# Performance work log

Measured on AMD Instinct MI355X. Metric: run time of the kernel, lower is better.

The kernel has to match this reference:

```python
import jax, jax.numpy as jnp
import numpy as np

B, N, N_IN, N_H = 8192, 16, 512, 256
NEG_ROUND = 1
MARGIN = 0.5
EPS = 1e-6  # torch F.pairwise_distance default eps


def setup_inputs() -> dict:
    key = jax.random.key(0)
    k0, k1, k2, k3 = jax.random.split(key, 4)
    seq1 = jax.random.normal(k0, (B, N, N_IN), dtype=jnp.float32)
    adj = jax.random.uniform(k1, (B, N, N), dtype=jnp.float32)
    # GCN linear (bias=False), xavier_uniform on [n_h, n_in] == same bound for [n_in, n_h]
    gx = float(np.sqrt(6.0 / (N_IN + N_H)))
    W_gcn = jax.random.uniform(k2, (N_IN, N_H), dtype=jnp.float32, minval=-gx, maxval=gx)
    b_gcn = jnp.zeros((N_H,), dtype=jnp.float32)  # Simple_GCN self.bias, init 0
    prelu_a = jnp.asarray(0.25, dtype=jnp.float32)  # nn.PReLU default
    bx = float(np.sqrt(6.0 / (N_H + N_H)))
    W_bil = jax.random.uniform(k3, (N_H, N_H), dtype=jnp.float32, minval=-bx, maxval=bx)
    b_bil = jnp.zeros((), dtype=jnp.float32)
    return {"seq1": seq1, "adj": adj, "W_gcn": W_gcn, "b_gcn": b_gcn,
            "prelu_a": prelu_a, "W_bil": W_bil, "b_bil": b_bil}


def reference(seq1, adj, W_gcn, b_gcn, prelu_a, W_bil, b_bil):
    # Simple_GCN: linear -> adjacency aggregate -> bias -> PReLU
    seq_fts = jnp.einsum('bnf,fh->bnh', seq1, W_gcn)           # [B,N,n_h]
    h1 = jnp.einsum('bnm,bmh->bnh', adj, seq_fts) + b_gcn      # bmm(adj, seq_fts)+bias
    h1 = jnp.where(h1 >= 0, h1, prelu_a * h1)                  # PReLU

    # avg readout over context nodes; last node is the target
    c = jnp.mean(h1[:, :-1, :], axis=1)                        # [B,n_h]
    h_mv = h1[:, -1, :]                                        # [B,n_h]

    def bilinear(x1, x2):  # nn.Bilinear(n_h, n_h, 1)
        return jnp.einsum('bi,ij,bj->b', x1, W_bil, x2)[:, None] + b_bil  # [B,1]

    scs = [bilinear(h_mv, c)]
    c_mi = c
    for _ in range(NEG_ROUND):  # fixed small loop, mirrors torch shift
        c_mi = jnp.concatenate([c_mi[-2:-1, :], c_mi[:-1, :]], axis=0)
        scs.append(bilinear(h_mv, c_mi))

    pos_dis = jnp.linalg.norm(h_mv - c + EPS, axis=-1)         # F.pairwise_distance
    neg_dis = jnp.linalg.norm(h_mv - c_mi + EPS, axis=-1)

    logits = jnp.concatenate(scs, axis=0)                      # [(1+NEG)*B, 1]
    # MarginRankingLoss(margin, reduction='none') with y=-1:
    # max(0, -y*(x1-x2)+margin) = max(0, (pos-neg)+margin)
    loss2 = jnp.maximum(0.0, (pos_dis - neg_dis) + MARGIN)     # [B]
    return (logits, loss2)
```

## Files before the change

kernel.cpp:

```cpp
#include <hip/hip_runtime.h>
#include <stdint.h>

typedef float f32x4 __attribute__((ext_vector_type(4)));
typedef __bf16 bfrag __attribute__((ext_vector_type(8)));
typedef unsigned short us4 __attribute__((ext_vector_type(4)));

__device__ __forceinline__ unsigned short f2bf(float f) {
  unsigned u = __float_as_uint(f);
  u += 0x7fff + ((u >> 16) & 1);
  return (unsigned short)(u >> 16);
}
__device__ __forceinline__ float bf2f(unsigned short s) {
  return __uint_as_float(((unsigned)s) << 16);
}

typedef __attribute__((address_space(3))) void lds_vp;
typedef __attribute__((address_space(1))) void gl_vp;
__device__ __forceinline__ void gload16(const void* g, void* l) {
  __builtin_amdgcn_global_load_lds((const gl_vp*)g, (lds_vp*)l, 16, 0, 0);
}

__global__ __launch_bounds__(256)
void conv_w_k(const float* __restrict__ Wg, const float* __restrict__ Wb,
              unsigned short* __restrict__ WgT, unsigned short* __restrict__ WbT) {
  int i = blockIdx.x * 256 + threadIdx.x;
  if (i < 512 * 256) { int k = i >> 8, c = i & 255; WgT[c * 512 + k] = f2bf(Wg[i]); }
  if (i < 256 * 256) { int k = i >> 8, c = i & 255; WbT[c * 256 + k] = f2bf(Wb[i]); }
}

__global__ __launch_bounds__(512, 4)
void fused1_k(const float* __restrict__ A, const unsigned short* __restrict__ Bt,
              const float* __restrict__ adj, const float* __restrict__ b_gcn,
              const float* __restrict__ prelu_a,
              float* __restrict__ Cout, float* __restrict__ Hmv) {
  __shared__ __align__(16) char sm[65536];
  const int t = threadIdx.x;
  const int lane = t & 63;
  const int wid = t >> 6;
  const int wm = wid >> 2, wn = wid & 3;
  const int lrow = lane & 15, lgrp = lane >> 4;
  const int wg = blockIdx.x;

  const float* gA = A + (size_t)(wg * 128 + (t >> 2)) * 512 + (t & 3) * 8;
  const int aw_off = t * 16;

  int aoff[4], boff[4];
#pragma unroll
  for (int m = 0; m < 4; m++) {
    int arow = wm * 64 + m * 16 + lrow;
    aoff[m] = arow * 64 + lgrp * 16;
  }
#pragma unroll
  for (int n = 0; n < 4; n++) {
    int bcol = wn * 64 + n * 16 + lrow;
    boff[n] = 8192 + bcol * 64 + ((lgrp ^ ((bcol ^ (bcol >> 2)) & 3)) << 4);
  }

  f32x4 acc[4][4];
#pragma unroll
  for (int m = 0; m < 4; m++)
#pragma unroll
    for (int n = 0; n < 4; n++) acc[m][n] = (f32x4)0.0f;

#define STAGE_B(buf, kc)                                                       \
  {                                                                            \
    _Pragma("unroll")                                                          \
    for (int i = 0; i < 2; i++) {                                              \
      int c = i * 512 + t;                                                     \
      int col = c >> 2, s = c & 3;                                             \
      int sp = s ^ ((col ^ (col >> 2)) & 3);                                   \
      gload16(Bt + (size_t)col * 512 + (kc) * 32 + sp * 8, (buf) + 8192 + c * 16); \
    }                                                                          \
  }

#define COMPUTE(cur)                                                           \
  {                                                                            \
    bfrag bf[4], af[4];                                                        \
    _Pragma("unroll")                                                          \
    for (int n = 0; n < 4; n++) bf[n] = *(const bfrag*)((cur) + boff[n]);      \
    _Pragma("unroll")                                                          \
    for (int m = 0; m < 4; m++) af[m] = *(const bfrag*)((cur) + aoff[m]);      \
    _Pragma("unroll")                                                          \
    for (int m = 0; m < 4; m++)                                                \
      _Pragma("unroll")                                                        \
      for (int n = 0; n < 4; n++)                                              \
        acc[m][n] = __builtin_amdgcn_mfma_f32_16x16x32_bf16(af[m], bf[n], acc[m][n], 0, 0, 0); \
  }

  {
    STAGE_B(sm, 0);
    f32x4 a0 = *(const f32x4*)(gA);
    f32x4 a1 = *(const f32x4*)(gA + 4);
    bfrag w;
    w[0] = (__bf16)a0.x; w[1] = (__bf16)a0.y; w[2] = (__bf16)a0.z; w[3] = (__bf16)a0.w;
    w[4] = (__bf16)a1.x; w[5] = (__bf16)a1.y; w[6] = (__bf16)a1.z; w[7] = (__bf16)a1.w;
    *(bfrag*)(sm + aw_off) = w;
    asm volatile("s_waitcnt vmcnt(0)" ::: "memory");
    asm volatile("s_waitcnt lgkmcnt(0)" ::: "memory");
    __builtin_amdgcn_s_barrier();
    asm volatile("" ::: "memory");
  }

  for (int kc = 0; kc < 15; ++kc) {
    char* cur = sm + (kc & 1) * 24576;
    char* nxt = sm + ((kc + 1) & 1) * 24576;
    f32x4 a0 = *(const f32x4*)(gA + (kc + 1) * 32);
    f32x4 a1 = *(const f32x4*)(gA + (kc + 1) * 32 + 4);
    STAGE_B(nxt, kc + 1);

    COMPUTE(cur);

    bfrag w;
    w[0] = (__bf16)a0.x; w[1] = (__bf16)a0.y; w[2] = (__bf16)a0.z; w[3] = (__bf16)a0.w;
    w[4] = (__bf16)a1.x; w[5] = (__bf16)a1.y; w[6] = (__bf16)a1.z; w[7] = (__bf16)a1.w;
    *(bfrag*)(nxt + aw_off) = w;
    asm volatile("s_waitcnt vmcnt(0)" ::: "memory");
    asm volatile("s_waitcnt lgkmcnt(0)" ::: "memory");
    __builtin_amdgcn_s_barrier();
    asm volatile("" ::: "memory");
  }
  COMPUTE(sm + 24576);
  __builtin_amdgcn_s_barrier();
  asm volatile("" ::: "memory");
#undef STAGE_B
#undef COMPUTE

  unsigned short* sf = (unsigned short*)sm;
#pragma unroll
  for (int m = 0; m < 4; m++) {
    int row = wm * 64 + m * 16 + lgrp * 4;
#pragma unroll
    for (int n = 0; n < 4; n++) {
      int col = wn * 64 + n * 16 + lrow;
#pragma unroll
      for (int rr = 0; rr < 4; rr++)
        sf[(row + rr) * 256 + col] = f2bf(acc[m][n][rr]);
    }
  }
  asm volatile("s_waitcnt lgkmcnt(0)" ::: "memory");
  __builtin_amdgcn_s_barrier();
  asm volatile("" ::: "memory");

  const float pa = prelu_a[0];
  const f32x4 bg = *(const f32x4*)(b_gcn + lane * 4);
  f32x4 sfr[16];
#pragma unroll
  for (int mm = 0; mm < 16; mm++) {
    us4 q = *(const us4*)(sf + (wid * 16 + mm) * 256 + lane * 4);
    f32x4 v;
    v.x = bf2f(q.x); v.y = bf2f(q.y); v.z = bf2f(q.z); v.w = bf2f(q.w);
    sfr[mm] = v;
  }
  const int b = wg * 8 + wid;
  const float* adjb = adj + (size_t)b * 256;
  f32x4 cacc = (f32x4)0.0f;
  f32x4 hmv = (f32x4)0.0f;
#pragma unroll
  for (int n = 0; n < 16; n++) {
    f32x4 a4 = (f32x4)0.0f;
#pragma unroll
    for (int m = 0; m < 16; m++) a4 += adjb[n * 16 + m] * sfr[m];
    a4 += bg;
    f32x4 hv;
    hv.x = a4.x >= 0.f ? a4.x : pa * a4.x;
    hv.y = a4.y >= 0.f ? a4.y : pa * a4.y;
    hv.z = a4.z >= 0.f ? a4.z : pa * a4.z;
    hv.w = a4.w >= 0.f ? a4.w : pa * a4.w;
    if (n < 15) cacc += hv; else hmv = hv;
  }
  cacc *= (1.0f / 15.0f);
  *(f32x4*)(Cout + (size_t)b * 256 + lane * 4) = cacc;
  *(f32x4*)(Hmv + (size_t)b * 256 + lane * 4) = hmv;
}

__device__ __forceinline__ void stage2(const float* __restrict__ A,
                                       const unsigned short* __restrict__ Bt,
                                       char* buf, int wg, int kc, int t) {
  {
    int c = t & 255;
    int row = c >> 3, s = c & 7;
    int sp = s ^ (((row & 3) << 1) | ((row >> 2) & 1));
    gload16(A + (size_t)(wg * 32 + row) * 256 + kc * 32 + sp * 4, buf + c * 16);
  }
#pragma unroll
  for (int i = 0; i < 2; i++) {
    int c = i * 512 + t;
    int col = c >> 2, s = c & 3;
    int sp = s ^ ((col ^ (col >> 2)) & 3);
    gload16(Bt + (size_t)col * 256 + kc * 32 + sp * 8, buf + 4096 + c * 16);
  }
}

__global__ __launch_bounds__(512)
void fused2_k(const float* __restrict__ A, const unsigned short* __restrict__ Bt,
              const float* __restrict__ C, const float* __restrict__ Hmv,
              const float* __restrict__ b_bil, float* __restrict__ out) {
  __shared__ __align__(16) char sm2[40960];
  const int t = threadIdx.x;
  const int lane = t & 63;
  const int wid = t >> 6;
  const int wm = wid >> 2, wn = wid & 3;
  const int lrow = lane & 15, lgrp = lane >> 4;
  const int wg = blockIdx.x;

  f32x4 acc[4];
#pragma unroll
  for (int n = 0; n < 4; n++) acc[n] = (f32x4)0.0f;

  stage2(A, Bt, sm2, wg, 0, t);

  for (int kc = 0; kc < 8; ++kc) {
    char* cur = sm2 + (kc & 1) * 20480;
    if (kc + 1 < 8) {
      stage2(A, Bt, sm2 + ((kc + 1) & 1) * 20480, wg, kc + 1, t);
      asm volatile("s_waitcnt vmcnt(3)" ::: "memory");
    } else {
      asm volatile("s_waitcnt vmcnt(0)" ::: "memory");
    }
    __builtin_amdgcn_s_barrier();
    asm volatile("" ::: "memory");

    bfrag bf[4];
#pragma unroll
    for (int n = 0; n < 4; n++) {
      int bcol = wn * 64 + n * 16 + lrow;
      int sB = (bcol ^ (bcol >> 2)) & 3;
      bf[n] = *(const bfrag*)(cur + 4096 + bcol * 64 + ((lgrp ^ sB) << 4));
    }
    {
      int arow = wm * 16 + lrow;
      int sw = ((arow & 3) << 1) | ((arow >> 2) & 1);
      f32x4 lo = *(const f32x4*)(cur + arow * 128 + (((lgrp * 2) ^ sw) << 4));
      f32x4 hi = *(const f32x4*)(cur + arow * 128 + (((lgrp * 2 + 1) ^ sw) << 4));
      bfrag am;
      am[0] = (__bf16)lo.x; am[1] = (__bf16)lo.y; am[2] = (__bf16)lo.z; am[3] = (__bf16)lo.w;
      am[4] = (__bf16)hi.x; am[5] = (__bf16)hi.y; am[6] = (__bf16)hi.z; am[7] = (__bf16)hi.w;
#pragma unroll
      for (int n = 0; n < 4; n++)
        acc[n] = __builtin_amdgcn_mfma_f32_16x16x32_bf16(am, bf[n], acc[n], 0, 0, 0);
    }
    __builtin_amdgcn_s_barrier();
    asm volatile("" ::: "memory");
  }

  float* sf = (float*)sm2;
  {
    int row = wm * 16 + lgrp * 4;
#pragma unroll
    for (int n = 0; n < 4; n++) {
      int col = wn * 64 + n * 16 + lrow;
#pragma unroll
      for (int rr = 0; rr < 4; rr++)
        sf[(row + rr) * 256 + col] = acc[n][rr];
    }
  }
  asm volatile("s_waitcnt lgkmcnt(0)" ::: "memory");
  __builtin_amdgcn_s_barrier();
  asm volatile("" ::: "memory");

  const float bb = b_bil[0];
#pragma unroll
  for (int r = 0; r < 4; ++r) {
    const int row = wid * 4 + r;
    const int b = wg * 32 + row;
    const int bp = (b == 0) ? 8190 : (b - 1);
    f32x4 tv = *(const f32x4*)(sf + row * 256 + lane * 4);
    f32x4 cv = *(const f32x4*)(C + (size_t)b * 256 + lane * 4);
    f32x4 cp = *(const f32x4*)(C + (size_t)bp * 256 + lane * 4);
    f32x4 hv = *(const f32x4*)(Hmv + (size_t)b * 256 + lane * 4);
    f32x4 d0 = hv - cv + 1e-6f;
    f32x4 d1 = hv - cp + 1e-6f;
    float s0 = tv.x * cv.x + tv.y * cv.y + tv.z * cv.z + tv.w * cv.w;
    float s1 = tv.x * cp.x + tv.y * cp.y + tv.z * cp.z + tv.w * cp.w;
    float p = d0.x * d0.x + d0.y * d0.y + d0.z * d0.z + d0.w * d0.w;
    float q = d1.x * d1.x + d1.y * d1.y + d1.z * d1.z + d1.w * d1.w;
#pragma unroll
    for (int m = 1; m < 64; m <<= 1) {
      s0 += __shfl_xor(s0, m, 64);
      s1 += __shfl_xor(s1, m, 64);
      p  += __shfl_xor(p, m, 64);
      q  += __shfl_xor(q, m, 64);
    }
    if (lane == 0) {
      out[b] = s0 + bb;
      out[8192 + b] = s1 + bb;
      out[16384 + b] = fmaxf(0.0f, sqrtf(p) - sqrtf(q) + 0.5f);
    }
  }
}

extern "C" void kernel_launch(void* const* d_in, const int* in_sizes, int n_in,
                              void* d_out, int out_size, void* d_ws, size_t ws_size,
                              hipStream_t stream) {
  (void)in_sizes; (void)n_in; (void)out_size; (void)ws_size;
  const float* seq1 = (const float*)d_in[0];
  const float* adj  = (const float*)d_in[1];
  const float* Wg   = (const float*)d_in[2];
  const float* bg   = (const float*)d_in[3];
  const float* pa   = (const float*)d_in[4];
  const float* Wb   = (const float*)d_in[5];
  const float* bb   = (const float*)d_in[6];
  float* out = (float*)d_out;
  char* ws = (char*)d_ws;

  unsigned short* WgT = (unsigned short*)(ws);
  unsigned short* WbT = (unsigned short*)(ws + 262144);
  float* C   = (float*)(ws + 524288);
  float* HMV = (float*)(ws + 524288 + 8388608);

  hipLaunchKernelGGL(conv_w_k, dim3(512), dim3(256), 0, stream, Wg, Wb, WgT, WbT);
  hipLaunchKernelGGL(fused1_k, dim3(1024), dim3(512), 0, stream,
                     seq1, WgT, adj, bg, pa, C, HMV);
  hipLaunchKernelGGL(fused2_k, dim3(256), dim3(512), 0, stream,
                     HMV, WbT, C, HMV, bb, out);
}
```

Before: 102.0 us.

## Enlarge GEMM tile to 256 rows with triple-buffered async fp32 A staging

The first fused kernel now handles 256 rows (16 batches) per block instead of 128. The fp32 activation tile is loaded straight into LDS with async global-to-LDS copies and converted to bf16 at fragment-read time, replacing register-staged conversion. A three-buffer pipeline with partial vmcnt waits replaces the double buffer that drained every iteration, and each wave computes a 64x128 tile, which raises MFMA work per B-fragment load. The cost is 144KB of dynamic shared memory, so only one block fits per CU and far fewer blocks are resident; the per-wave accumulators also double, which adds register pressure.

```diff
diff --git a/kernel.cpp b/kernel.cpp
--- a/kernel.cpp
+++ b/kernel.cpp
@@ -28,101 +28,104 @@
   if (i < 256 * 256) { int k = i >> 8, c = i & 255; WbT[c * 256 + k] = f2bf(Wb[i]); }
 }
 
-__global__ __launch_bounds__(512, 4)
+__global__ __launch_bounds__(512)
 void fused1_k(const float* __restrict__ A, const unsigned short* __restrict__ Bt,
               const float* __restrict__ adj, const float* __restrict__ b_gcn,
               const float* __restrict__ prelu_a,
               float* __restrict__ Cout, float* __restrict__ Hmv) {
-  __shared__ __align__(16) char sm[65536];
+  extern __shared__ __align__(16) char sm[];
   const int t = threadIdx.x;
   const int lane = t & 63;
   const int wid = t >> 6;
-  const int wm = wid >> 2, wn = wid & 3;
+  const int wm = wid >> 1, wn = wid & 1;
   const int lrow = lane & 15, lgrp = lane >> 4;
   const int wg = blockIdx.x;
 
-  const float* gA = A + (size_t)(wg * 128 + (t >> 2)) * 512 + (t & 3) * 8;
-  const int aw_off = t * 16;
-
-  int aoff[4], boff[4];
+  int aoff0[4], aoff1[4], boff[8];
 #pragma unroll
   for (int m = 0; m < 4; m++) {
     int arow = wm * 64 + m * 16 + lrow;
-    aoff[m] = arow * 64 + lgrp * 16;
-  }
-#pragma unroll
-  for (int n = 0; n < 4; n++) {
-    int bcol = wn * 64 + n * 16 + lrow;
-    boff[n] = 8192 + bcol * 64 + ((lgrp ^ ((bcol ^ (bcol >> 2)) & 3)) << 4);
-  }
-
-  f32x4 acc[4][4];
+    int s0 = (2 * lgrp) ^ (arow & 7);
+    int s1 = (2 * lgrp + 1) ^ (arow & 7);
+    aoff0[m] = arow * 128 + (s0 << 4);
+    aoff1[m] = arow * 128 + (s1 << 4);
+  }
+#pragma unroll
+  for (int n = 0; n < 8; n++) {
+    int bcol = wn * 128 + n * 16 + lrow;
+    boff[n] = 32768 + bcol * 64 + ((lgrp ^ ((bcol ^ (bcol >> 2)) & 3)) << 4);
+  }
+
+  f32x4 acc[4][8];
 #pragma unroll
   for (int m = 0; m < 4; m++)
 #pragma unroll
-    for (int n = 0; n < 4; n++) acc[m][n] = (f32x4)0.0f;
-
-#define STAGE_B(buf, kc)                                                       \
+    for (int n = 0; n < 8; n++) acc[m][n] = (f32x4)0.0f;
+
+#define STAGE(bufidx, kc)                                                      \
   {                                                                            \
     _Pragma("unroll")                                                          \
-    for (int i = 0; i < 2; i++) {                                              \
+    for (int i = 0; i < 4; i++) {             \
+      int c = i * 512 + t;                                                     \
+      int row = c >> 3, s = c & 7;                                             \
+      int sp = s ^ (row & 7);                                                  \
+      gload16(A + (size_t)(wg * 256 + row) * 512 + (kc) * 32 + sp * 4,         \
+              sm + (bufidx) * 49152 + c * 16);                                 \
+    }                                                                          \
+    _Pragma("unroll")                                                          \
+    for (int i = 0; i < 2; i++) {            \
       int c = i * 512 + t;                                                     \
       int col = c >> 2, s = c & 3;                                             \
       int sp = s ^ ((col ^ (col >> 2)) & 3);                                   \
-      gload16(Bt + (size_t)col * 512 + (kc) * 32 + sp * 8, (buf) + 8192 + c * 16); \
+      gload16(Bt + (size_t)col * 512 + (kc) * 32 + sp * 8,                     \
+              sm + (bufidx) * 49152 + 32768 + c * 16);                         \
     }                                                                          \
   }
 
-#define COMPUTE(cur)                                                           \
+#define COMPUTE(bufidx)                                                        \
   {                                                                            \
-    bfrag bf[4], af[4];                                                        \
+    const char* cur = sm + (bufidx) * 49152;                                   \
+    bfrag bf[8];                                                               \
     _Pragma("unroll")                                                          \
-    for (int n = 0; n < 4; n++) bf[n] = *(const bfrag*)((cur) + boff[n]);      \
+    for (int n = 0; n < 8; n++) bf[n] = *(const bfrag*)(cur + boff[n]);        \
     _Pragma("unroll")                                                          \
-    for (int m = 0; m < 4; m++) af[m] = *(const bfrag*)((cur) + aoff[m]);      \
-    _Pragma("unroll")                                                          \
-    for (int m = 0; m < 4; m++)                                                \
+    for (int m = 0; m < 4; m++) {                                              \
+      f32x4 lo = *(const f32x4*)(cur + aoff0[m]);                              \
+      f32x4 hi = *(const f32x4*)(cur + aoff1[m]);                              \
+      bfrag am;                                                                \
+      am[0] = (__bf16)lo.x; am[1] = (__bf16)lo.y;                              \
+      am[2] = (__bf16)lo.z; am[3] = (__bf16)lo.w;                              \
+      am[4] = (__bf16)hi.x; am[5] = (__bf16)hi.y;                              \
+      am[6] = (__bf16)hi.z; am[7] = (__bf16)hi.w;                              \
       _Pragma("unroll")                                                        \
-      for (int n = 0; n < 4; n++)                                              \
-        acc[m][n] = __builtin_amdgcn_mfma_f32_16x16x32_bf16(af[m], bf[n], acc[m][n], 0, 0, 0); \
-  }
-
-  {
-    STAGE_B(sm, 0);
-    f32x4 a0 = *(const f32x4*)(gA);
-    f32x4 a1 = *(const f32x4*)(gA + 4);
-    bfrag w;
-    w[0] = (__bf16)a0.x; w[1] = (__bf16)a0.y; w[2] = (__bf16)a0.z; w[3] = (__bf16)a0.w;
-    w[4] = (__bf16)a1.x; w[5] = (__bf16)a1.y; w[6] = (__bf16)a1.z; w[7] = (__bf16)a1.w;
-    *(bfrag*)(sm + aw_off) = w;
-    asm volatile("s_waitcnt vmcnt(0)" ::: "memory");
-    asm volatile("s_waitcnt lgkmcnt(0)" ::: "memory");
+      for (int n = 0; n < 8; n++)                                              \
+        acc[m][n] = __builtin_amdgcn_mfma_f32_16x16x32_bf16(am, bf[n], acc[m][n], 0, 0, 0); \
+    }                                                                          \
+  }
+
+  STAGE(0, 0);
+  STAGE(1, 1);
+  asm volatile("s_waitcnt vmcnt(6)" ::: "memory");
+  __builtin_amdgcn_s_barrier();
+  asm volatile("" ::: "memory");
+
+#pragma unroll
+  for (int p = 0; p < 16; ++p) {
+    if (p < 14) {
+      STAGE((p + 2) % 3, p + 2);
+      asm volatile("s_waitcnt vmcnt(12)" ::: "memory");
+    } else if (p == 14) {
+      asm volatile("s_waitcnt vmcnt(6)" ::: "memory");
+    } else {
+      asm volatile("s_waitcnt vmcnt(0)" ::: "memory");
+    }
     __builtin_amdgcn_s_barrier();
     asm volatile("" ::: "memory");
-  }
-
-  for (int kc = 0; kc < 15; ++kc) {
-    char* cur = sm + (kc & 1) * 24576;
-    char* nxt = sm + ((kc + 1) & 1) * 24576;
-    f32x4 a0 = *(const f32x4*)(gA + (kc + 1) * 32);
-    f32x4 a1 = *(const f32x4*)(gA + (kc + 1) * 32 + 4);
-    STAGE_B(nxt, kc + 1);
-
-    COMPUTE(cur);
-
-    bfrag w;
-    w[0] = (__bf16)a0.x; w[1] = (__bf16)a0.y; w[2] = (__bf16)a0.z; w[3] = (__bf16)a0.w;
-    w[4] = (__bf16)a1.x; w[5] = (__bf16)a1.y; w[6] = (__bf16)a1.z; w[7] = (__bf16)a1.w;
-    *(bfrag*)(nxt + aw_off) = w;
-    asm volatile("s_waitcnt vmcnt(0)" ::: "memory");
-    asm volatile("s_waitcnt lgkmcnt(0)" ::: "memory");
+    COMPUTE(p % 3);
     __builtin_amdgcn_s_barrier();
     asm volatile("" ::: "memory");
   }
-  COMPUTE(sm + 24576);
-  __builtin_amdgcn_s_barrier();
-  asm volatile("" ::: "memory");
-#undef STAGE_B
+#undef STAGE
 #undef COMPUTE
 
   unsigned short* sf = (unsigned short*)sm;
@@ -130,8 +133,8 @@
   for (int m = 0; m < 4; m++) {
     int row = wm * 64 + m * 16 + lgrp * 4;
 #pragma unroll
-    for (int n = 0; n < 4; n++) {
-      int col = wn * 64 + n * 16 + lrow;
+    for (int n = 0; n < 8; n++) {
+      int col = wn * 128 + n * 16 + lrow;
 #pragma unroll
       for (int rr = 0; rr < 4; rr++)
         sf[(row + rr) * 256 + col] = f2bf(acc[m][n][rr]);
@@ -143,34 +146,38 @@
 
   const float pa = prelu_a[0];
   const f32x4 bg = *(const f32x4*)(b_gcn + lane * 4);
-  f32x4 sfr[16];
-#pragma unroll
-  for (int mm = 0; mm < 16; mm++) {
-    us4 q = *(const us4*)(sf + (wid * 16 + mm) * 256 + lane * 4);
-    f32x4 v;
-    v.x = bf2f(q.x); v.y = bf2f(q.y); v.z = bf2f(q.z); v.w = bf2f(q.w);
-    sfr[mm] = v;
-  }
-  const int b = wg * 8 + wid;
-  const float* adjb = adj + (size_t)b * 256;
-  f32x4 cacc = (f32x4)0.0f;
-  f32x4 hmv = (f32x4)0.0f;
-#pragma unroll
-  for (int n = 0; n < 16; n++) {
-    f32x4 a4 = (f32x4)0.0f;
-#pragma unroll
-    for (int m = 0; m < 16; m++) a4 += adjb[n * 16 + m] * sfr[m];
-    a4 += bg;
-    f32x4 hv;
-    hv.x = a4.x >= 0.f ? a4.x : pa * a4.x;
-    hv.y = a4.y >= 0.f ? a4.y : pa * a4.y;
-    hv.z = a4.z >= 0.f ? a4.z : pa * a4.z;
-    hv.w = a4.w >= 0.f ? a4.w : pa * a4.w;
-    if (n < 15) cacc += hv; else hmv = hv;
-  }
-  cacc *= (1.0f / 15.0f);
-  *(f32x4*)(Cout + (size_t)b * 256 + lane * 4) = cacc;
-  *(f32x4*)(Hmv + (size_t)b * 256 + lane * 4) = hmv;
+#pragma unroll
+  for (int lb = 0; lb < 2; ++lb) {
+    const int lbat = wid * 2 + lb;
+    f32x4 sfr[16];
+#pragma unroll
+    for (int mm = 0; mm < 16; mm++) {
+      us4 q = *(const us4*)(sf + (lbat * 16 + mm) * 256 + lane * 4);
+      f32x4 v;
+      v.x = bf2f(q.x); v.y = bf2f(q.y); v.z = bf2f(q.z); v.w = bf2f(q.w);
+      sfr[mm] = v;
+    }
+    const int b = wg * 16 + lbat;
+    const float* adjb = adj + (size_t)b * 256;
+    f32x4 cacc = (f32x4)0.0f;
+    f32x4 hmv = (f32x4)0.0f;
+#pragma unroll
+    for (int n = 0; n < 16; n++) {
+      f32x4 a4 = (f32x4)0.0f;
+#pragma unroll
+      for (int m = 0; m < 16; m++) a4 += adjb[n * 16 + m] * sfr[m];
+      a4 += bg;
+      f32x4 hv;
+      hv.x = a4.x >= 0.f ? a4.x : pa * a4.x;
+      hv.y = a4.y >= 0.f ? a4.y : pa * a4.y;
+      hv.z = a4.z >= 0.f ? a4.z : pa * a4.z;
+      hv.w = a4.w >= 0.f ? a4.w : pa * a4.w;
+      if (n < 15) cacc += hv; else hmv = hv;
+    }
+    cacc *= (1.0f / 15.0f);
+    *(f32x4*)(Cout + (size_t)b * 256 + lane * 4) = cacc;
+    *(f32x4*)(Hmv + (size_t)b * 256 + lane * 4) = hmv;
+  }
 }
 
 __device__ __forceinline__ void stage2(const float* __restrict__ A,
@@ -308,8 +315,11 @@
   float* C   = (float*)(ws + 524288);
   float* HMV = (float*)(ws + 524288 + 8388608);
 
+  (void)hipFuncSetAttribute((const void*)fused1_k,
+                            hipFuncAttributeMaxDynamicSharedMemorySize, 147456);
+
   hipLaunchKernelGGL(conv_w_k, dim3(512), dim3(256), 0, stream, Wg, Wb, WgT, WbT);
-  hipLaunchKernelGGL(fused1_k, dim3(1024), dim3(512), 0, stream,
+  hipLaunchKernelGGL(fused1_k, dim3(512), dim3(512), 147456, stream,
                      seq1, WgT, adj, bg, pa, C, HMV);
   hipLaunchKernelGGL(fused2_k, dim3(256), dim3(512), 0, stream,
                      HMV, WbT, C, HMV, bb, out);
```

After: 133.7 us. 1.31x slower.
